# Kernel tuning notes

Measured on AMD Instinct MI355X. Metric: run time of the kernel, lower is better.

Reference implementation:

```python
import jax, jax.numpy as jnp
import numpy as np

B, T, E = 2, 2048, 4096
HQ, HKV = 32, 8
D = E // HQ          # 128 head dim
G = HQ // HKV        # 4 groups


def _apply_rope(x, fr):
    # x: [B,H,T,D]; fr: [T, D/2, 2] (cos, sin)
    x = x.reshape(*x.shape[:-1], -1, 2)
    c, s = fr[..., 0], fr[..., 1]
    y = jnp.stack([x[..., 0] * c - x[..., 1] * s,
                   x[..., 1] * c + x[..., 0] * s], axis=-1)
    return y.reshape(*y.shape[:-2], -1)


def setup_inputs() -> dict:
    key = jax.random.key(0)
    ks = jax.random.split(key, 8)
    query = jax.random.normal(ks[0], (B, T, E), jnp.float32)
    kin = jax.random.normal(ks[1], (B, T, E), jnp.float32)
    vin = jax.random.normal(ks[2], (B, T, E), jnp.float32)
    s = 1.0 / np.sqrt(E)
    Wq = jax.random.normal(ks[3], (E, E), jnp.float32) * s
    Wk = jax.random.normal(ks[4], (HKV * D, E), jnp.float32) * s
    Wv = jax.random.normal(ks[5], (HKV * D, E), jnp.float32) * s
    Wo = jax.random.normal(ks[6], (E, E), jnp.float32) * s
    bq = jnp.zeros((E,), jnp.float32)
    bk = jnp.zeros((HKV * D,), jnp.float32)
    bv = jnp.zeros((HKV * D,), jnp.float32)
    bo = jnp.zeros((E,), jnp.float32)
    # standard RoPE table: [T, D/2, 2] = (cos, sin)
    inv_freq = 1.0 / (10000.0 ** (np.arange(0, D, 2, dtype=np.float32) / D))
    ang = np.outer(np.arange(T, dtype=np.float32), inv_freq)  # [T, D/2]
    freqs_cis_real_and_imag = jnp.asarray(
        np.stack([np.cos(ang), np.sin(ang)], axis=-1), jnp.float32)
    mask = jnp.tril(jnp.ones((1, 1, T, T), jnp.int32))  # causal
    return {"query": query, "key": kin, "value": vin,
            "freqs_cis_real_and_imag": freqs_cis_real_and_imag, "mask": mask,
            "Wq": Wq, "bq": bq, "Wk": Wk, "bk": bk,
            "Wv": Wv, "bv": bv, "Wo": Wo, "bo": bo}


def reference(query, key, value, freqs_cis_real_and_imag, mask,
              Wq, bq, Wk, bk, Wv, bv, Wo, bo):
    Bsz, Tlen, _ = query.shape
    Q = (query @ Wq.T + bq).reshape(Bsz, Tlen, HQ, D).transpose(0, 2, 1, 3)
    K = (key @ Wk.T + bk).reshape(Bsz, Tlen, HKV, D).transpose(0, 2, 1, 3)
    V = (value @ Wv.T + bv).reshape(Bsz, Tlen, HKV, D).transpose(0, 2, 1, 3)
    # GQA: expand kv heads to query heads (repeat_interleave on head dim)
    K = jnp.repeat(K, G, axis=1)
    V = jnp.repeat(V, G, axis=1)
    fr = freqs_cis_real_and_imag[:Tlen]
    Q = _apply_rope(Q, fr)
    K = _apply_rope(K, fr)
    score = jnp.einsum('bhqd,bhkd->bhqk', Q, K) / jnp.sqrt(jnp.float32(D))
    score = jnp.where(mask == 0, -jnp.inf, score)
    w = jax.nn.softmax(score, axis=-1)
    y = jnp.einsum('bhqk,bhkd->bhqd', w, V)
    y = y.transpose(0, 2, 1, 3).reshape(Bsz, Tlen, HQ * D)
    return y @ Wo.T + bo  # dropout: eval mode (identity)
```

## Files before the change

### kernel.cpp

```cpp
#include <hip/hip_runtime.h>
#include <hip/hip_bf16.h>

typedef __attribute__((ext_vector_type(4))) float f32x4;
typedef __attribute__((ext_vector_type(8))) short bf16x8;
typedef __attribute__((ext_vector_type(4))) short bf16x4;

#define MFMA16(a,b,c) __builtin_amdgcn_mfma_f32_16x16x32_bf16(a,b,c,0,0,0)
#define GLLDS16(g, l) __builtin_amdgcn_global_load_lds( \
    (const __attribute__((address_space(1))) unsigned int*)(g), \
    (__attribute__((address_space(3))) unsigned int*)(l), 16, 0, 0)

constexpr int BATCH = 2, SEQ = 2048, EMB = 4096;
constexpr int NHQ = 32, NHKV = 8, HD = 128, GRP = 4;

static __device__ __forceinline__ short f2bf(float f) {
    union { float f; unsigned u; } v; v.f = f;
    unsigned r = v.u + 0x7fff + ((v.u >> 16) & 1);
    return (short)(r >> 16);
}
static __device__ __forceinline__ bf16x8 cvt8(f32x4 a, f32x4 b) {
    bf16x8 r;
    r[0]=f2bf(a[0]); r[1]=f2bf(a[1]); r[2]=f2bf(a[2]); r[3]=f2bf(a[3]);
    r[4]=f2bf(b[0]); r[5]=f2bf(b[1]); r[6]=f2bf(b[2]); r[7]=f2bf(b[3]);
    return r;
}

__global__ __launch_bounds__(256) void cvt_bf16(
    const float* __restrict__ src, short* __restrict__ dst, int n8)
{
    int i = blockIdx.x * blockDim.x + threadIdx.x;
    const int stride = gridDim.x * blockDim.x;
    for (; i < n8; i += stride) {
        f32x4 a = *(const f32x4*)(src + (size_t)i * 8);
        f32x4 b = *(const f32x4*)(src + (size_t)i * 8 + 4);
        *(bf16x8*)(dst + (size_t)i * 8) = cvt8(a, b);
    }
}

template<int MODE>
__global__ __launch_bounds__(256) void gemm_bt(
    const short* __restrict__ A, const short* __restrict__ W,
    const float* __restrict__ bias, const float* __restrict__ freqs,
    void* __restrict__ outv, int M, int N, int K, int NH)
{
    __shared__ short As[128][64];
    __shared__ short Bs[128][64];

    const int tid = threadIdx.x;
    const int lane = tid & 63, wave = tid >> 6;
    const int ln = lane & 15, quad = lane >> 4;
    const int wm = wave >> 1, wn = wave & 1;
    const int rowbase = blockIdx.y * 128;
    const int colbase = blockIdx.x * 128;

    f32x4 acc[4][4];
#pragma unroll
    for (int i = 0; i < 4; i++)
#pragma unroll
        for (int j = 0; j < 4; j++) acc[i][j] = (f32x4){0.f, 0.f, 0.f, 0.f};

    for (int kk = 0; kk < K; kk += 64) {
        __syncthreads();
#pragma unroll
        for (int i = 0; i < 4; ++i) {
            const int row = wave * 32 + i * 8;
            const short* g = A + (size_t)(rowbase + row + (lane >> 3)) * K + kk + (lane & 7) * 8;
            GLLDS16(g, &As[row][0]);
        }
#pragma unroll
        for (int i = 0; i < 4; ++i) {
            const int row = wave * 32 + i * 8;
            const short* g = W + (size_t)(colbase + row + (lane >> 3)) * K + kk + (lane & 7) * 8;
            GLLDS16(g, &Bs[row][0]);
        }
        __syncthreads();

#pragma unroll
        for (int kc = 0; kc < 2; ++kc) {
            bf16x8 af[4], bfr[4];
#pragma unroll
            for (int i = 0; i < 4; i++)
                af[i] = *(const bf16x8*)&As[wm * 64 + i * 16 + ln][kc * 32 + quad * 8];
#pragma unroll
            for (int i = 0; i < 4; i++)
                bfr[i] = *(const bf16x8*)&Bs[wn * 64 + i * 16 + ln][kc * 32 + quad * 8];
#pragma unroll
            for (int i = 0; i < 4; i++)
#pragma unroll
                for (int j = 0; j < 4; j++)
                    acc[i][j] = MFMA16(af[i], bfr[j], acc[i][j]);
        }
    }

#pragma unroll
    for (int i = 0; i < 4; i++) {
        const int r0 = rowbase + wm * 64 + i * 16 + quad * 4;
#pragma unroll
        for (int j = 0; j < 4; j++) {
            const int c = colbase + wn * 64 + j * 16 + ln;
            const float bv = bias[c];
            if (MODE == 0) {
                float* out = (float*)outv;
#pragma unroll
                for (int rg = 0; rg < 4; rg++)
                    out[(size_t)(r0 + rg) * N + c] = acc[i][j][rg] + bv;
            } else if (MODE == 1) {
                short* out = (short*)outv;
                const int h = c / HD, d = c % HD;
#pragma unroll
                for (int rg = 0; rg < 4; rg++) {
                    const int r = r0 + rg;
                    const int bb = r / SEQ, t = r % SEQ;
                    const float v = acc[i][j][rg] + bv;
                    const float p = __shfl_xor(v, 1);
                    const int fi = (t * (HD / 2) + (d >> 1)) * 2;
                    const float co = freqs[fi], si = freqs[fi + 1];
                    const float y = (d & 1) ? (v * co + p * si) : (v * co - p * si);
                    out[(((size_t)bb * NH + h) * SEQ + t) * HD + d] = f2bf(y);
                }
            } else {
                short* out = (short*)outv;
                const int h = c / HD, d = c % HD;
                const int bb = r0 / SEQ, t0 = r0 % SEQ;
                bf16x4 pk;
#pragma unroll
                for (int rg = 0; rg < 4; rg++) pk[rg] = f2bf(acc[i][j][rg] + bv);
                *(bf16x4*)(out + (((size_t)bb * NHKV + h) * HD + d) * SEQ + t0) = pk;
            }
        }
    }
}

__global__ __launch_bounds__(256) void attn(
    const short* __restrict__ Qr, const short* __restrict__ Kr,
    const short* __restrict__ Vt, short* __restrict__ Y)
{
    __shared__ short Ks[64][128];
    __shared__ short Vs[128][64];
    __shared__ short Ps[4][16][80];

    const int tid = threadIdx.x;
    const int lane = tid & 63, wave = tid >> 6;
    const int ln = lane & 15, quad = lane >> 4;
    const int qt = (int)gridDim.x - 1 - (int)blockIdx.x;
    const int kvh = blockIdx.y, b = blockIdx.z;
    const int h = kvh * GRP + wave;
    const int qbase = qt * 32;
    const int sx = (ln & 7) << 3;

    const short* Qh = Qr + (((size_t)b * NHQ + h) * SEQ + qbase) * HD;
    const short* Kh = Kr + ((size_t)b * NHKV + kvh) * SEQ * HD;
    const short* Vh = Vt + ((size_t)b * NHKV + kvh) * (size_t)HD * SEQ;

    bf16x8 aQ[2][4];
#pragma unroll
    for (int mi = 0; mi < 2; mi++)
#pragma unroll
        for (int dc = 0; dc < 4; dc++)
            aQ[mi][dc] = *(const bf16x8*)(Qh + (size_t)(mi * 16 + ln) * HD + dc * 32 + quad * 8);

    f32x4 oa[2][8];
#pragma unroll
    for (int mi = 0; mi < 2; mi++)
#pragma unroll
        for (int dt = 0; dt < 8; dt++) oa[mi][dt] = (f32x4){0.f, 0.f, 0.f, 0.f};
    float mrun[2][4], lrun[2][4];
#pragma unroll
    for (int mi = 0; mi < 2; mi++)
#pragma unroll
        for (int rg = 0; rg < 4; rg++) { mrun[mi][rg] = -INFINITY; lrun[mi][rg] = 0.f; }

    const int nkt = (qbase + 95) >> 6;
    for (int kt = 0; kt < nkt; ++kt) {
        __syncthreads();
#pragma unroll
        for (int i = 0; i < 4; ++i) {
            const int row0 = wave * 16 + i * 4;
            const int rr = row0 + (lane >> 4);
            const short* g = Kh + (size_t)(kt * 64 + rr) * HD + (((lane & 15) ^ (rr & 7)) << 3);
            GLLDS16(g, &Ks[row0][0]);
        }
#pragma unroll
        for (int i = 0; i < 4; ++i) {
            const int row0 = wave * 32 + i * 8;
            const int rr = row0 + (lane >> 3);
            const short* g = Vh + (size_t)rr * SEQ + kt * 64 + (((lane & 7) ^ (lane >> 3)) << 3);
            GLLDS16(g, &Vs[row0][0]);
        }
        __syncthreads();

#pragma unroll
        for (int mi = 0; mi < 2; mi++) {
            float s[4][4];
#pragma unroll
            for (int nt = 0; nt < 4; nt++) {
                f32x4 sa = (f32x4){0.f, 0.f, 0.f, 0.f};
#pragma unroll
                for (int dc = 0; dc < 4; dc++) {
                    bf16x8 bK = *(const bf16x8*)&Ks[nt * 16 + ln][(dc * 32 + quad * 8) ^ sx];
                    sa = MFMA16(aQ[mi][dc], bK, sa);
                }
                const int kg = kt * 64 + nt * 16 + ln;
#pragma unroll
                for (int rg = 0; rg < 4; rg++) {
                    const int qg = qbase + mi * 16 + quad * 4 + rg;
                    s[nt][rg] = (kg <= qg) ? sa[rg] * 0.08838834764831845f : -INFINITY;
                }
            }
            float al[4];
#pragma unroll
            for (int rg = 0; rg < 4; rg++) {
                float mx = fmaxf(fmaxf(s[0][rg], s[1][rg]), fmaxf(s[2][rg], s[3][rg]));
                mx = fmaxf(mx, __shfl_xor(mx, 1));
                mx = fmaxf(mx, __shfl_xor(mx, 2));
                mx = fmaxf(mx, __shfl_xor(mx, 4));
                mx = fmaxf(mx, __shfl_xor(mx, 8));
                const float mnew = fmaxf(mrun[mi][rg], mx);
                const float a = __expf(mrun[mi][rg] - mnew);
                float rs = 0.f;
#pragma unroll
                for (int nt = 0; nt < 4; nt++) {
                    const float p = __expf(s[nt][rg] - mnew);
                    s[nt][rg] = p; rs += p;
                }
                rs += __shfl_xor(rs, 1); rs += __shfl_xor(rs, 2);
                rs += __shfl_xor(rs, 4); rs += __shfl_xor(rs, 8);
                lrun[mi][rg] = lrun[mi][rg] * a + rs;
                mrun[mi][rg] = mnew;
                al[rg] = a;
            }
#pragma unroll
            for (int dt = 0; dt < 8; dt++)
#pragma unroll
                for (int rg = 0; rg < 4; rg++) oa[mi][dt][rg] *= al[rg];
#pragma unroll
            for (int nt = 0; nt < 4; nt++)
#pragma unroll
                for (int rg = 0; rg < 4; rg++)
                    Ps[wave][quad * 4 + rg][nt * 16 + ln] = f2bf(s[nt][rg]);
#pragma unroll
            for (int kc = 0; kc < 2; kc++) {
                bf16x8 aP = *(const bf16x8*)&Ps[wave][ln][kc * 32 + quad * 8];
#pragma unroll
                for (int dt = 0; dt < 8; dt++) {
                    bf16x8 bV = *(const bf16x8*)&Vs[dt * 16 + ln][(kc * 32 + quad * 8) ^ sx];
                    oa[mi][dt] = MFMA16(aP, bV, oa[mi][dt]);
                }
            }
        }
    }

#pragma unroll
    for (int mi = 0; mi < 2; mi++) {
#pragma unroll
        for (int rg = 0; rg < 4; rg++) {
            const float inv = 1.f / lrun[mi][rg];
            const int t = qbase + mi * 16 + quad * 4 + rg;
            const size_t rowoff = ((size_t)b * SEQ + t) * EMB + h * HD;
#pragma unroll
            for (int dt = 0; dt < 8; dt++)
                Y[rowoff + dt * 16 + ln] = f2bf(oa[mi][dt][rg] * inv);
        }
    }
}

extern "C" void kernel_launch(void* const* d_in, const int* in_sizes, int n_in,
                              void* d_out, int out_size, void* d_ws, size_t ws_size,
                              hipStream_t stream) {
    const float* q  = (const float*)d_in[0];
    const float* k  = (const float*)d_in[1];
    const float* v  = (const float*)d_in[2];
    const float* fr = (const float*)d_in[3];
    const float* Wq = (const float*)d_in[5];
    const float* bq = (const float*)d_in[6];
    const float* Wk = (const float*)d_in[7];
    const float* bk = (const float*)d_in[8];
    const float* Wv = (const float*)d_in[9];
    const float* bv = (const float*)d_in[10];
    const float* Wo = (const float*)d_in[11];
    const float* bo = (const float*)d_in[12];

    char* ws = (char*)d_ws;
    short* Qr = (short*)(ws);
    short* Kr = (short*)(ws + 33554432);
    short* Vt = (short*)(ws + 41943040);
    short* Yb = (short*)(ws + 50331648);
    short* Wb = (short*)(ws + 83886080);
    float* out = (float*)d_out;

    const int M = BATCH * SEQ;
    dim3 blk(256);
    const int big8 = EMB * EMB / 8, small8 = NHKV * HD * EMB / 8, act8 = M * EMB / 8;

    cvt_bf16<<<1024, blk, 0, stream>>>(Wq, Wb, big8);
    cvt_bf16<<<1024, blk, 0, stream>>>(q, Yb, act8);
    gemm_bt<1><<<dim3(EMB / 128, M / 128), blk, 0, stream>>>(Yb, Wb, bq, fr, Qr, M, EMB, EMB, NHQ);
    cvt_bf16<<<1024, blk, 0, stream>>>(Wk, Wb, small8);
    cvt_bf16<<<1024, blk, 0, stream>>>(k, Yb, act8);
    gemm_bt<1><<<dim3((NHKV * HD) / 128, M / 128), blk, 0, stream>>>(Yb, Wb, bk, fr, Kr, M, NHKV * HD, EMB, NHKV);
    cvt_bf16<<<1024, blk, 0, stream>>>(Wv, Wb, small8);
    cvt_bf16<<<1024, blk, 0, stream>>>(v, Yb, act8);
    gemm_bt<2><<<dim3((NHKV * HD) / 128, M / 128), blk, 0, stream>>>(Yb, Wb, bv, nullptr, Vt, M, NHKV * HD, EMB, NHKV);
    attn<<<dim3(SEQ / 32, NHKV, BATCH), blk, 0, stream>>>(Qr, Kr, Vt, Yb);
    cvt_bf16<<<1024, blk, 0, stream>>>(Wo, Wb, big8);
    gemm_bt<0><<<dim3(EMB / 128, M / 128), blk, 0, stream>>>(Yb, Wb, bo, nullptr, out, M, EMB, EMB, 0);
}
```

Before: 1.284 ms.

## Double-buffer K/V tiles, add lazy softmax rescaling and MFMA priority hints

The attention kernel now keeps two LDS buffers for the K and V tiles and prefetches the next tile with global_load_lds while the current one is being computed. This removes one barrier per iteration and overlaps memory latency with the MFMA work. Online softmax rescaling of the accumulator is skipped unless some row's max grows by more than a threshold of 8, which cuts the per-tile multiplies. s_setprio is raised around the MFMA sections. The double buffer doubles the K/V LDS footprint, which may lower occupancy. The lazy rescale lets probabilities exceed 1 by up to e^8 before renormalisation.

```diff
diff --git a/kernel.cpp b/kernel.cpp
--- a/kernel.cpp
+++ b/kernel.cpp
@@ -135,8 +135,8 @@
     const short* __restrict__ Qr, const short* __restrict__ Kr,
     const short* __restrict__ Vt, short* __restrict__ Y)
 {
-    __shared__ short Ks[64][128];
-    __shared__ short Vs[128][64];
+    __shared__ short Ks[2][64][128];
+    __shared__ short Vs[2][128][64];
     __shared__ short Ps[4][16][80];
 
     const int tid = threadIdx.x;
@@ -152,52 +152,59 @@
     const short* Kh = Kr + ((size_t)b * NHKV + kvh) * SEQ * HD;
     const short* Vh = Vt + ((size_t)b * NHKV + kvh) * (size_t)HD * SEQ;
 
-    bf16x8 aQ[2][4];
-#pragma unroll
-    for (int mi = 0; mi < 2; mi++)
-#pragma unroll
-        for (int dc = 0; dc < 4; dc++)
-            aQ[mi][dc] = *(const bf16x8*)(Qh + (size_t)(mi * 16 + ln) * HD + dc * 32 + quad * 8);
-
-    f32x4 oa[2][8];
-#pragma unroll
-    for (int mi = 0; mi < 2; mi++)
-#pragma unroll
-        for (int dt = 0; dt < 8; dt++) oa[mi][dt] = (f32x4){0.f, 0.f, 0.f, 0.f};
-    float mrun[2][4], lrun[2][4];
-#pragma unroll
-    for (int mi = 0; mi < 2; mi++)
-#pragma unroll
-        for (int rg = 0; rg < 4; rg++) { mrun[mi][rg] = -INFINITY; lrun[mi][rg] = 0.f; }
-
-    const int nkt = (qbase + 95) >> 6;
-    for (int kt = 0; kt < nkt; ++kt) {
-        __syncthreads();
+    auto stage = [&](int bb, int kt) {
 #pragma unroll
         for (int i = 0; i < 4; ++i) {
             const int row0 = wave * 16 + i * 4;
             const int rr = row0 + (lane >> 4);
             const short* g = Kh + (size_t)(kt * 64 + rr) * HD + (((lane & 15) ^ (rr & 7)) << 3);
-            GLLDS16(g, &Ks[row0][0]);
+            GLLDS16(g, &Ks[bb][row0][0]);
         }
 #pragma unroll
         for (int i = 0; i < 4; ++i) {
             const int row0 = wave * 32 + i * 8;
             const int rr = row0 + (lane >> 3);
             const short* g = Vh + (size_t)rr * SEQ + kt * 64 + (((lane & 7) ^ (lane >> 3)) << 3);
-            GLLDS16(g, &Vs[row0][0]);
-        }
-        __syncthreads();
+            GLLDS16(g, &Vs[bb][row0][0]);
+        }
+    };
+
+    bf16x8 aQ[2][4];
+#pragma unroll
+    for (int mi = 0; mi < 2; mi++)
+#pragma unroll
+        for (int dc = 0; dc < 4; dc++)
+            aQ[mi][dc] = *(const bf16x8*)(Qh + (size_t)(mi * 16 + ln) * HD + dc * 32 + quad * 8);
+
+    f32x4 oa[2][8];
+#pragma unroll
+    for (int mi = 0; mi < 2; mi++)
+#pragma unroll
+        for (int dt = 0; dt < 8; dt++) oa[mi][dt] = (f32x4){0.f, 0.f, 0.f, 0.f};
+    float mrun[2][4], lrun[2][4];
+#pragma unroll
+    for (int mi = 0; mi < 2; mi++)
+#pragma unroll
+        for (int rg = 0; rg < 4; rg++) { mrun[mi][rg] = -INFINITY; lrun[mi][rg] = 0.f; }
+
+    const int nkt = (qbase + 95) >> 6;
+    stage(0, 0);
+    __syncthreads();
+    int cur = 0;
+
+    for (int kt = 0; kt < nkt; ++kt) {
+        if (kt + 1 < nkt) stage(cur ^ 1, kt + 1);
 
 #pragma unroll
         for (int mi = 0; mi < 2; mi++) {
             float s[4][4];
+            __builtin_amdgcn_s_setprio(1);
 #pragma unroll
             for (int nt = 0; nt < 4; nt++) {
                 f32x4 sa = (f32x4){0.f, 0.f, 0.f, 0.f};
 #pragma unroll
                 for (int dc = 0; dc < 4; dc++) {
-                    bf16x8 bK = *(const bf16x8*)&Ks[nt * 16 + ln][(dc * 32 + quad * 8) ^ sx];
+                    bf16x8 bK = *(const bf16x8*)&Ks[cur][nt * 16 + ln][(dc * 32 + quad * 8) ^ sx];
                     sa = MFMA16(aQ[mi][dc], bK, sa);
                 }
                 const int kg = kt * 64 + nt * 16 + ln;
@@ -207,7 +214,9 @@
                     s[nt][rg] = (kg <= qg) ? sa[rg] * 0.08838834764831845f : -INFINITY;
                 }
             }
-            float al[4];
+            __builtin_amdgcn_s_setprio(0);
+
+            float mx4[4];
 #pragma unroll
             for (int rg = 0; rg < 4; rg++) {
                 float mx = fmaxf(fmaxf(s[0][rg], s[1][rg]), fmaxf(s[2][rg], s[3][rg]));
@@ -215,39 +224,56 @@
                 mx = fmaxf(mx, __shfl_xor(mx, 2));
                 mx = fmaxf(mx, __shfl_xor(mx, 4));
                 mx = fmaxf(mx, __shfl_xor(mx, 8));
-                const float mnew = fmaxf(mrun[mi][rg], mx);
-                const float a = __expf(mrun[mi][rg] - mnew);
+                mx4[rg] = mx;
+            }
+            bool ok = (mx4[0] <= mrun[mi][0] + 8.f) & (mx4[1] <= mrun[mi][1] + 8.f) &
+                      (mx4[2] <= mrun[mi][2] + 8.f) & (mx4[3] <= mrun[mi][3] + 8.f);
+            if (!__all(ok)) {
+#pragma unroll
+                for (int rg = 0; rg < 4; rg++) {
+                    const float mnew = fmaxf(mrun[mi][rg], mx4[rg]);
+                    const float a = __expf(mrun[mi][rg] - mnew);
+                    mrun[mi][rg] = mnew;
+                    lrun[mi][rg] *= a;
+                    mx4[rg] = a;
+                }
+#pragma unroll
+                for (int dt = 0; dt < 8; dt++)
+#pragma unroll
+                    for (int rg = 0; rg < 4; rg++) oa[mi][dt][rg] *= mx4[rg];
+            }
+#pragma unroll
+            for (int rg = 0; rg < 4; rg++) {
                 float rs = 0.f;
 #pragma unroll
                 for (int nt = 0; nt < 4; nt++) {
-                    const float p = __expf(s[nt][rg] - mnew);
+                    const float p = __expf(s[nt][rg] - mrun[mi][rg]);
                     s[nt][rg] = p; rs += p;
                 }
                 rs += __shfl_xor(rs, 1); rs += __shfl_xor(rs, 2);
                 rs += __shfl_xor(rs, 4); rs += __shfl_xor(rs, 8);
-                lrun[mi][rg] = lrun[mi][rg] * a + rs;
-                mrun[mi][rg] = mnew;
-                al[rg] = a;
-            }
-#pragma unroll
-            for (int dt = 0; dt < 8; dt++)
-#pragma unroll
-                for (int rg = 0; rg < 4; rg++) oa[mi][dt][rg] *= al[rg];
+                lrun[mi][rg] += rs;
+            }
 #pragma unroll
             for (int nt = 0; nt < 4; nt++)
 #pragma unroll
                 for (int rg = 0; rg < 4; rg++)
                     Ps[wave][quad * 4 + rg][nt * 16 + ln] = f2bf(s[nt][rg]);
+            __builtin_amdgcn_s_setprio(1);
 #pragma unroll
             for (int kc = 0; kc < 2; kc++) {
                 bf16x8 aP = *(const bf16x8*)&Ps[wave][ln][kc * 32 + quad * 8];
 #pragma unroll
                 for (int dt = 0; dt < 8; dt++) {
-                    bf16x8 bV = *(const bf16x8*)&Vs[dt * 16 + ln][(kc * 32 + quad * 8) ^ sx];
+                    bf16x8 bV = *(const bf16x8*)&Vs[cur][dt * 16 + ln][(kc * 32 + quad * 8) ^ sx];
                     oa[mi][dt] = MFMA16(aP, bV, oa[mi][dt]);
                 }
             }
-        }
+            __builtin_amdgcn_s_setprio(0);
+        }
+
+        __syncthreads();
+        cur ^= 1;
     }
 
 #pragma unroll
```

After: 1.343 ms. 4.7% more time.
